# Optimization experiments

Hardware: AMD Instinct MI355X
Metric: run time of the kernel (lower is better)

## Reference

```python
import jax, jax.numpy as jnp
import numpy as np

N = 100000      # total nodes (herb + ingredient + target concatenated)
E = 1600000     # edges (all etypes concatenated)
D_IN = 128
D_HID = 128
D_OUT = 128
BN_EPS = 1e-5
LEAKY_SLOPE = 0.01


def setup_inputs() -> dict:
    key = jax.random.key(0)
    ks = jax.random.split(key, 8)
    x = jax.random.normal(ks[0], (N, D_IN), dtype=jnp.float32)
    src = jax.random.randint(ks[1], (E,), 0, N, dtype=jnp.int32)
    dst = jax.random.randint(ks[2], (E,), 0, N, dtype=jnp.int32)
    W1 = jax.random.normal(ks[3], (D_IN, D_HID), dtype=jnp.float32) * (1.0 / np.sqrt(D_IN))
    b1 = jnp.zeros((D_HID,), jnp.float32)
    W2 = jax.random.normal(ks[4], (D_HID, D_OUT), dtype=jnp.float32) * (1.0 / np.sqrt(D_HID))
    b2 = jnp.zeros((D_OUT,), jnp.float32)
    gamma = jnp.ones((D_HID,), jnp.float32)
    beta = jnp.zeros((D_HID,), jnp.float32)
    run_mean = jax.random.normal(ks[5], (D_HID,), jnp.float32) * 0.1
    run_var = jax.random.uniform(ks[6], (D_HID,), jnp.float32, 0.5, 1.5)
    return {"x": x, "src": src, "dst": dst, "W1": W1, "b1": b1,
            "W2": W2, "b2": b2, "gamma": gamma, "beta": beta,
            "run_mean": run_mean, "run_var": run_var}


def _graph_conv(h, s, d, W, b, norm_src, norm_dst):
    # DGL GraphConv, norm='both': D_out^{-1/2} then sum-aggregate then D_in^{-1/2}, then linear
    h = h * norm_src                                   # [N, d]
    m = jax.ops.segment_sum(h[s], d, num_segments=N)   # gather + spmm-aggregate
    m = m * norm_dst
    return m @ W + b


def reference(x, src, dst, W1, b1, W2, b2, gamma, beta, run_mean, run_var):
    # dgl.add_self_loop: append (i, i) for every node
    loop = jnp.arange(N, dtype=src.dtype)
    s = jnp.concatenate([src, loop])
    d = jnp.concatenate([dst, loop])
    ones = jnp.ones(s.shape[0], jnp.float32)
    out_deg = jnp.maximum(jax.ops.segment_sum(ones, s, num_segments=N), 1.0)
    in_deg = jnp.maximum(jax.ops.segment_sum(ones, d, num_segments=N), 1.0)
    norm_src = (out_deg ** -0.5)[:, None]
    norm_dst = (in_deg ** -0.5)[:, None]

    # layer 0: conv -> BN (eval, running stats) -> leaky_relu -> dropout (eval = identity)
    h = _graph_conv(x, s, d, W1, b1, norm_src, norm_dst)
    h = (h - run_mean) * jax.lax.rsqrt(run_var + BN_EPS) * gamma + beta
    h = jnp.where(h > 0, h, LEAKY_SLOPE * h)

    # layer 1 (last): conv only
    h = _graph_conv(h, s, d, W2, b2, norm_src, norm_dst)
    return h
```

## Files before the change

### kernel.cpp

```cpp
#include <hip/hip_runtime.h>

#define NN 100000
#define NE 1600000
#define D 128
#define LEAKY 0.01f
#define BNEPS 1e-5f

#define G 256
#define CHUNK 6250
#define B 782
#define BSHIFT 7
#define BMASK 127
#define NXCD 8

typedef short v8s __attribute__((ext_vector_type(8)));
typedef float v4f __attribute__((ext_vector_type(4)));

__device__ __forceinline__ unsigned f2bf(float f) {
    unsigned u = __float_as_uint(f);
    return (u + 0x7fffu + ((u >> 16) & 1u)) >> 16;
}
__device__ __forceinline__ float bf2f(unsigned h) {
    return __uint_as_float(h << 16);
}

__device__ __forceinline__ int xcc_id() {
    int x;
    asm volatile("s_getreg_b32 %0, hwreg(HW_REG_XCC_ID)" : "=s"(x));
    return x & (NXCD - 1);
}


__global__ __launch_bounds__(1024) void hist_kernel(const int* __restrict__ src,
                                                    const int* __restrict__ dst,
                                                    int* __restrict__ degP,
                                                    int* __restrict__ hist) {
    __shared__ int h[B];
    for (int i = threadIdx.x; i < B; i += 1024) h[i] = 0;
    __syncthreads();
    int g = blockIdx.x;
    int* dp0 = (int*)(degP) + (size_t)xcc_id() * NN;
    const int* dp = dst + g * CHUNK;
    const int* sp = src + g * CHUNK;
    for (int k = threadIdx.x; k < CHUNK; k += 1024) {
        atomicAdd(&h[dp[k] >> BSHIFT], 1);
        __hip_atomic_fetch_add(&dp0[sp[k]], 1, __ATOMIC_RELAXED,
                               __HIP_MEMORY_SCOPE_WORKGROUP);
    }
    __syncthreads();
    for (int i = threadIdx.x; i < B; i += 1024) hist[i * G + g] = h[i];
}

__global__ void scanA(const int* __restrict__ a, int* __restrict__ bsum) {
    __shared__ int sm[256];
    int t = threadIdx.x;
    sm[t] = a[blockIdx.x * 256 + t];
    __syncthreads();
    for (int s = 128; s > 0; s >>= 1) {
        if (t < s) sm[t] += sm[t + s];
        __syncthreads();
    }
    if (t == 0) bsum[blockIdx.x] = sm[0];
}

__global__ void scanB(const int* __restrict__ bsum, int* __restrict__ boffs) {
    int lane = threadIdx.x;
    int run = 0;
    for (int base = 0; base < B; base += 64) {
        int i = base + lane;
        int v = (i < B) ? bsum[i] : 0;
        int orig = v;
        for (int off = 1; off < 64; off <<= 1) {
            int t = __shfl_up(v, off);
            if (lane >= off) v += t;
        }
        if (i < B) boffs[i] = run + v - orig;
        run += __shfl(v, 63);
    }
}

__global__ void scanC(const int* __restrict__ a, const int* __restrict__ boffs,
                      int* __restrict__ offs) {
    __shared__ int sm[256];
    int t = threadIdx.x;
    int i = blockIdx.x * 256 + t;
    int v = a[i];
    sm[t] = v;
    __syncthreads();
    for (int off = 1; off < 256; off <<= 1) {
        int x = (t >= off) ? sm[t - off] : 0;
        __syncthreads();
        sm[t] += x;
        __syncthreads();
    }
    offs[i] = boffs[blockIdx.x] + sm[t] - v;
}

__global__ __launch_bounds__(1024) void sort_kernel(const int* __restrict__ src,
                                                    const int* __restrict__ dst,
                                                    const int* __restrict__ offs,
                                                    unsigned* __restrict__ ebuf) {
    __shared__ int cur[B];
    int g = blockIdx.x;
    for (int i = threadIdx.x; i < B; i += 1024) cur[i] = offs[i * G + g];
    __syncthreads();
    const int* sp = src + g * CHUNK;
    const int* dp = dst + g * CHUNK;
    for (int k = threadIdx.x; k < CHUNK; k += 1024) {
        int d = dp[k], s = sp[k];
        int pos = atomicAdd(&cur[d >> BSHIFT], 1);
        ebuf[pos] = ((unsigned)(d & BMASK) << 17) | (unsigned)s;
    }
}


__global__ __launch_bounds__(256) void conv_kernel(const float* __restrict__ x,
                                                   const int* __restrict__ degP,
                                                   float* __restrict__ norm_s,
                                                   unsigned* __restrict__ hb) {
    int t = blockIdx.x * 256 + threadIdx.x;
    if (t >= NN * 64) return;
    int row = t >> 6;
    int dsum = 0;
    #pragma unroll
    for (int p = 0; p < NXCD; ++p) dsum += degP[(size_t)p * NN + row];
    float ns = rsqrtf((float)(dsum + 1));
    if ((t & 63) == 0) norm_s[row] = ns;
    float2 v = ((const float2*)x)[t];
    hb[t] = f2bf(v.x * ns) | (f2bf(v.y * ns) << 16);
}


__global__ __launch_bounds__(256) void local_sort(
    const int* __restrict__ offs, unsigned* __restrict__ ebuf,
    int* __restrict__ row, float* __restrict__ norm_d)
{
    __shared__ int cnt[128];
    __shared__ int sc[128];
    const int b = blockIdx.x;
    const int t = threadIdx.x;
    const int s = offs[b * G];
    const int e = (b == B - 1) ? NE : offs[(b + 1) * G];
    if (t < 128) cnt[t] = 0;
    __syncthreads();

    unsigned ent[16];
    int nent = 0;
    for (int k = s + t; k < e && nent < 16; k += 256) {
        unsigned u = ebuf[k];
        ent[nent++] = u;
        atomicAdd(&cnt[u >> 17], 1);
    }
    __syncthreads();

    if (t < 128) sc[t] = cnt[t];
    __syncthreads();
    for (int off = 1; off < 128; off <<= 1) {
        int v = 0;
        if (t < 128 && t >= off) v = sc[t - off];
        __syncthreads();
        if (t < 128) sc[t] += v;
        __syncthreads();
    }
    if (t < 128) {
        int st = s + sc[t] - cnt[t];
        int node = b * 128 + t;
        if (node < NN) {
            row[node] = st;
            norm_d[node] = rsqrtf((float)(cnt[t] + 1));
        }
        cnt[t] = st;
    }
    if (b == B - 1 && t == 0) row[NN] = NE;
    __syncthreads();

    for (int i = 0; i < nent; ++i) {
        unsigned u = ent[i];
        int pos = atomicAdd(&cnt[u >> 17], 1);
        ebuf[pos] = u & 0x1FFFFu;
    }
}


__global__ __launch_bounds__(256) void csr_agg(
    const int* __restrict__ row, const int* __restrict__ csr,
    const unsigned* __restrict__ hp,
    unsigned* __restrict__ Ahi, unsigned* __restrict__ Alo)
{
    int i = blockIdx.x * 4 + (threadIdx.x >> 6);
    if (i >= NN) return;
    int lane = threadIdx.x & 63;

    float2 acc;
    {
        unsigned u = hp[(size_t)i * 64 + lane];
        acc.x = __uint_as_float(u << 16);
        acc.y = __uint_as_float(u & 0xffff0000u);
    }

    int start = row[i], end = row[i + 1];
    for (int base = start; base < end; base += 64) {
        int n = end - base; if (n > 64) n = 64;
        int sv = csr[base + (lane < n ? lane : n - 1)];
        int j = 0;
        for (; j + 8 <= n; j += 8) {
            int ss[8]; unsigned uu[8];
            #pragma unroll
            for (int t = 0; t < 8; ++t) ss[t] = __shfl(sv, j + t);
            #pragma unroll
            for (int t = 0; t < 8; ++t) uu[t] = hp[(size_t)ss[t] * 64 + lane];
            #pragma unroll
            for (int t = 0; t < 8; ++t) {
                acc.x += __uint_as_float(uu[t] << 16);
                acc.y += __uint_as_float(uu[t] & 0xffff0000u);
            }
        }
        for (; j < n; ++j) {
            int s = __shfl(sv, j);
            unsigned u = hp[(size_t)s * 64 + lane];
            acc.x += __uint_as_float(u << 16);
            acc.y += __uint_as_float(u & 0xffff0000u);
        }
    }
    unsigned hx = f2bf(acc.x), hy = f2bf(acc.y);
    float lx = acc.x - bf2f(hx), ly = acc.y - bf2f(hy);
    Ahi[(size_t)i * 64 + lane] = hx | (hy << 16);
    Alo[(size_t)i * 64 + lane] = f2bf(lx) | (f2bf(ly) << 16);
}


template<bool LAYER0>
__global__ __launch_bounds__(256) void gemm_kernel(
    const unsigned* __restrict__ Ahi_g, const unsigned* __restrict__ Alo_g,
    const float* __restrict__ W, const float* __restrict__ bias,
    const float* __restrict__ norm_s, const float* __restrict__ norm_d,
    const float* __restrict__ gamma, const float* __restrict__ beta,
    const float* __restrict__ rmean, const float* __restrict__ rvar,
    float* __restrict__ outf, unsigned short* __restrict__ outb)
{
    __shared__ unsigned lhi[64 * 68];
    __shared__ unsigned llo[64 * 68];

    const int w    = threadIdx.x >> 6;
    const int lane = threadIdx.x & 63;
    const int quad = lane >> 4;
    const int l16  = lane & 15;

    v8s Bhi[2][4], Blo[2][4];
    int col[2];
    #pragma unroll
    for (int ct = 0; ct < 2; ++ct) {
        col[ct] = 32 * w + 16 * ct + l16;
        #pragma unroll
        for (int q = 0; q < 4; ++q) {
            int kb = 32 * q + quad * 8;
            v8s hi8, lo8;
            #pragma unroll
            for (int kk = 0; kk < 8; ++kk) {
                float wv = W[(kb + kk) * D + col[ct]];
                unsigned h = f2bf(wv);
                hi8[kk] = (short)h;
                lo8[kk] = (short)f2bf(wv - bf2f(h));
            }
            Bhi[ct][q] = hi8;
            Blo[ct][q] = lo8;
        }
    }

    float bcol[2], s[2] = {0.f, 0.f}, sh[2] = {0.f, 0.f};
    #pragma unroll
    for (int ct = 0; ct < 2; ++ct) {
        bcol[ct] = bias[col[ct]];
        if (LAYER0) {
            s[ct]  = gamma[col[ct]] * rsqrtf(rvar[col[ct]] + BNEPS);
            sh[ct] = beta[col[ct]] - rmean[col[ct]] * s[ct];
        }
    }

    for (int row0 = blockIdx.x * 64; row0 < NN; row0 += gridDim.x * 64) {
        __syncthreads();
        for (int idx = threadIdx.x; idx < 64 * 64; idx += 256) {
            int r = idx >> 6, cp = idx & 63;
            int rw = row0 + r;
            unsigned vh = 0, vl = 0;
            if (rw < NN) {
                vh = Ahi_g[(size_t)rw * 64 + cp];
                vl = Alo_g[(size_t)rw * 64 + cp];
            }
            lhi[r * 68 + cp] = vh;
            llo[r * 68 + cp] = vl;
        }
        __syncthreads();

        #pragma unroll
        for (int rt = 0; rt < 4; ++rt) {
            v4f acc0 = {0.f, 0.f, 0.f, 0.f};
            v4f acc1 = {0.f, 0.f, 0.f, 0.f};
            #pragma unroll
            for (int q = 0; q < 4; ++q) {
                const unsigned short* ph = (const unsigned short*)lhi
                    + (rt * 16 + l16) * 136 + q * 32 + quad * 8;
                const unsigned short* pl = (const unsigned short*)llo
                    + (rt * 16 + l16) * 136 + q * 32 + quad * 8;
                v8s ahi = *(const v8s*)ph;
                v8s alo = *(const v8s*)pl;
                acc0 = __builtin_amdgcn_mfma_f32_16x16x32_bf16(ahi, Bhi[0][q], acc0, 0, 0, 0);
                acc0 = __builtin_amdgcn_mfma_f32_16x16x32_bf16(alo, Bhi[0][q], acc0, 0, 0, 0);
                acc0 = __builtin_amdgcn_mfma_f32_16x16x32_bf16(ahi, Blo[0][q], acc0, 0, 0, 0);
                acc1 = __builtin_amdgcn_mfma_f32_16x16x32_bf16(ahi, Bhi[1][q], acc1, 0, 0, 0);
                acc1 = __builtin_amdgcn_mfma_f32_16x16x32_bf16(alo, Bhi[1][q], acc1, 0, 0, 0);
                acc1 = __builtin_amdgcn_mfma_f32_16x16x32_bf16(ahi, Blo[1][q], acc1, 0, 0, 0);
            }
            #pragma unroll
            for (int r = 0; r < 4; ++r) {
                int rw = row0 + rt * 16 + quad * 4 + r;
                if (rw >= NN) continue;
                float nd = norm_d[rw];
                float o0 = acc0[r] * nd + bcol[0];
                float o1 = acc1[r] * nd + bcol[1];
                if (LAYER0) {
                    o0 = o0 * s[0] + sh[0];
                    o1 = o1 * s[1] + sh[1];
                    o0 = o0 > 0.f ? o0 : LEAKY * o0;
                    o1 = o1 > 0.f ? o1 : LEAKY * o1;
                    float ns = norm_s[rw];
                    o0 *= ns; o1 *= ns;
                    outb[(size_t)rw * D + col[0]] = (unsigned short)f2bf(o0);
                    outb[(size_t)rw * D + col[1]] = (unsigned short)f2bf(o1);
                } else {
                    outf[(size_t)rw * D + col[0]] = o0;
                    outf[(size_t)rw * D + col[1]] = o1;
                }
            }
        }
    }
}


extern "C" void kernel_launch(void* const* d_in, const int* in_sizes, int n_in,
                              void* d_out, int out_size, void* d_ws, size_t ws_size,
                              hipStream_t stream) {
    const float* x     = (const float*)d_in[0];
    const int*   src   = (const int*)d_in[1];
    const int*   dst   = (const int*)d_in[2];
    const float* W1    = (const float*)d_in[3];
    const float* b1    = (const float*)d_in[4];
    const float* W2    = (const float*)d_in[5];
    const float* b2    = (const float*)d_in[6];
    const float* gamma = (const float*)d_in[7];
    const float* beta  = (const float*)d_in[8];
    const float* rmean = (const float*)d_in[9];
    const float* rvar  = (const float*)d_in[10];
    float* out = (float*)d_out;

    unsigned* hb = (unsigned*)d_out;

    unsigned* Ahi   = (unsigned*)d_ws;
    unsigned* Alo   = Ahi + (size_t)NN * 64;
    float*    norm  = (float*)(Alo + (size_t)NN * 64);
    int*      deg   = (int*)(norm + 2 * NN);
    int*      hist  = deg + NN;
    int*      offs  = hist + B * G;
    int*      bsum  = offs + B * G;
    int*      boffs = bsum + B;
    unsigned* ebuf  = (unsigned*)(boffs + B);
    float* norm_s = norm;
    float* norm_d = norm + NN;
    int*   row    = hist;

    int* degP = (int*)Ahi;

    hipMemsetAsync(degP, 0, (size_t)NXCD * NN * sizeof(int), stream);

    hist_kernel<<<G, 1024, 0, stream>>>(src, dst, degP, hist);
    scanA<<<B * G / 256, 256, 0, stream>>>(hist, bsum);
    scanB<<<1, 64, 0, stream>>>(bsum, boffs);
    scanC<<<B * G / 256, 256, 0, stream>>>(hist, boffs, offs);
    sort_kernel<<<G, 1024, 0, stream>>>(src, dst, offs, ebuf);
    conv_kernel<<<(NN * 64 + 255) / 256, 256, 0, stream>>>(x, degP, norm_s, hb);
    local_sort<<<B, 256, 0, stream>>>(offs, ebuf, row, norm_d);

    const int AGG_BLOCKS = (NN + 3) / 4;
    const int GEMM_BLOCKS = 784;
    csr_agg<<<AGG_BLOCKS, 256, 0, stream>>>(row, (const int*)ebuf, hb, Ahi, Alo);
    gemm_kernel<true><<<GEMM_BLOCKS, 256, 0, stream>>>(Ahi, Alo, W1, b1,
                                                       norm_s, norm_d,
                                                       gamma, beta, rmean, rvar,
                                                       nullptr, (unsigned short*)hb);
    csr_agg<<<AGG_BLOCKS, 256, 0, stream>>>(row, (const int*)ebuf, hb, Ahi, Alo);
    gemm_kernel<false><<<GEMM_BLOCKS, 256, 0, stream>>>(Ahi, Alo, W2, b2,
                                                        norm_s, norm_d,
                                                        nullptr, nullptr, nullptr, nullptr,
                                                        out, nullptr);
}
```

Measured before the change: 454.2 us.

## Fuse CSR aggregation into GEMM kernel, keeping aggregated rows in LDS

Merges the CSR gather-aggregate and the MFMA GEMM into one kernel per layer. Each block aggregates 64 destination rows, with each wave handling 16 rows in sequence, and writes the hi/lo bf16 split straight into shared memory instead of global Ahi/Alo buffers. This removes the global write and re-read of the aggregated matrix and two kernel launches. In exchange, parallelism per row drops (one wave serially handles 16 rows), the per-block W conversion now runs once per 64 rows, and a slow wave with high-degree rows can stall the whole block at the barrier.

```diff
diff --git a/kernel.cpp b/kernel.cpp
--- a/kernel.cpp
+++ b/kernel.cpp
@@ -182,56 +182,10 @@
 }
 
 
-__global__ __launch_bounds__(256) void csr_agg(
-    const int* __restrict__ row, const int* __restrict__ csr,
+template<bool LAYER0>
+__global__ __launch_bounds__(256) void fused_kernel(
+    const int* __restrict__ rowp, const int* __restrict__ csr,
     const unsigned* __restrict__ hp,
-    unsigned* __restrict__ Ahi, unsigned* __restrict__ Alo)
-{
-    int i = blockIdx.x * 4 + (threadIdx.x >> 6);
-    if (i >= NN) return;
-    int lane = threadIdx.x & 63;
-
-    float2 acc;
-    {
-        unsigned u = hp[(size_t)i * 64 + lane];
-        acc.x = __uint_as_float(u << 16);
-        acc.y = __uint_as_float(u & 0xffff0000u);
-    }
-
-    int start = row[i], end = row[i + 1];
-    for (int base = start; base < end; base += 64) {
-        int n = end - base; if (n > 64) n = 64;
-        int sv = csr[base + (lane < n ? lane : n - 1)];
-        int j = 0;
-        for (; j + 8 <= n; j += 8) {
-            int ss[8]; unsigned uu[8];
-            #pragma unroll
-            for (int t = 0; t < 8; ++t) ss[t] = __shfl(sv, j + t);
-            #pragma unroll
-            for (int t = 0; t < 8; ++t) uu[t] = hp[(size_t)ss[t] * 64 + lane];
-            #pragma unroll
-            for (int t = 0; t < 8; ++t) {
-                acc.x += __uint_as_float(uu[t] << 16);
-                acc.y += __uint_as_float(uu[t] & 0xffff0000u);
-            }
-        }
-        for (; j < n; ++j) {
-            int s = __shfl(sv, j);
-            unsigned u = hp[(size_t)s * 64 + lane];
-            acc.x += __uint_as_float(u << 16);
-            acc.y += __uint_as_float(u & 0xffff0000u);
-        }
-    }
-    unsigned hx = f2bf(acc.x), hy = f2bf(acc.y);
-    float lx = acc.x - bf2f(hx), ly = acc.y - bf2f(hy);
-    Ahi[(size_t)i * 64 + lane] = hx | (hy << 16);
-    Alo[(size_t)i * 64 + lane] = f2bf(lx) | (f2bf(ly) << 16);
-}
-
-
-template<bool LAYER0>
-__global__ __launch_bounds__(256) void gemm_kernel(
-    const unsigned* __restrict__ Ahi_g, const unsigned* __restrict__ Alo_g,
     const float* __restrict__ W, const float* __restrict__ bias,
     const float* __restrict__ norm_s, const float* __restrict__ norm_d,
     const float* __restrict__ gamma, const float* __restrict__ beta,
@@ -245,6 +199,7 @@
     const int lane = threadIdx.x & 63;
     const int quad = lane >> 4;
     const int l16  = lane & 15;
+    const int row0 = blockIdx.x * 64;
 
     v8s Bhi[2][4], Blo[2][4];
     int col[2];
@@ -277,60 +232,84 @@
         }
     }
 
-    for (int row0 = blockIdx.x * 64; row0 < NN; row0 += gridDim.x * 64) {
-        __syncthreads();
-        for (int idx = threadIdx.x; idx < 64 * 64; idx += 256) {
-            int r = idx >> 6, cp = idx & 63;
-            int rw = row0 + r;
-            unsigned vh = 0, vl = 0;
-            if (rw < NN) {
-                vh = Ahi_g[(size_t)rw * 64 + cp];
-                vl = Alo_g[(size_t)rw * 64 + cp];
+    for (int k16 = 0; k16 < 16; ++k16) {
+        const int r = w * 16 + k16;
+        const int i = row0 + r;
+        float2 acc = {0.f, 0.f};
+        if (i < NN) {
+            unsigned u = hp[(size_t)i * 64 + lane];
+            acc.x = __uint_as_float(u << 16);
+            acc.y = __uint_as_float(u & 0xffff0000u);
+            int start = rowp[i], end = rowp[i + 1];
+            for (int base = start; base < end; base += 64) {
+                int n = end - base; if (n > 64) n = 64;
+                int sv = csr[base + (lane < n ? lane : n - 1)];
+                int j = 0;
+                for (; j + 8 <= n; j += 8) {
+                    int ss[8]; unsigned uu[8];
+                    #pragma unroll
+                    for (int t = 0; t < 8; ++t) ss[t] = __shfl(sv, j + t);
+                    #pragma unroll
+                    for (int t = 0; t < 8; ++t) uu[t] = hp[(size_t)ss[t] * 64 + lane];
+                    #pragma unroll
+                    for (int t = 0; t < 8; ++t) {
+                        acc.x += __uint_as_float(uu[t] << 16);
+                        acc.y += __uint_as_float(uu[t] & 0xffff0000u);
+                    }
+                }
+                for (; j < n; ++j) {
+                    int sidx = __shfl(sv, j);
+                    unsigned u2 = hp[(size_t)sidx * 64 + lane];
+                    acc.x += __uint_as_float(u2 << 16);
+                    acc.y += __uint_as_float(u2 & 0xffff0000u);
+                }
             }
-            lhi[r * 68 + cp] = vh;
-            llo[r * 68 + cp] = vl;
-        }
-        __syncthreads();
-
+        }
+        unsigned hx = f2bf(acc.x), hy = f2bf(acc.y);
+        float lx = acc.x - bf2f(hx), ly = acc.y - bf2f(hy);
+        lhi[r * 68 + lane] = hx | (hy << 16);
+        llo[r * 68 + lane] = f2bf(lx) | (f2bf(ly) << 16);
+    }
+    __syncthreads();
+
+    #pragma unroll
+    for (int rt = 0; rt < 4; ++rt) {
+        v4f acc0 = {0.f, 0.f, 0.f, 0.f};
+        v4f acc1 = {0.f, 0.f, 0.f, 0.f};
         #pragma unroll
-        for (int rt = 0; rt < 4; ++rt) {
-            v4f acc0 = {0.f, 0.f, 0.f, 0.f};
-            v4f acc1 = {0.f, 0.f, 0.f, 0.f};
-            #pragma unroll
-            for (int q = 0; q < 4; ++q) {
-                const unsigned short* ph = (const unsigned short*)lhi
-                    + (rt * 16 + l16) * 136 + q * 32 + quad * 8;
-                const unsigned short* pl = (const unsigned short*)llo
-                    + (rt * 16 + l16) * 136 + q * 32 + quad * 8;
-                v8s ahi = *(const v8s*)ph;
-                v8s alo = *(const v8s*)pl;
-                acc0 = __builtin_amdgcn_mfma_f32_16x16x32_bf16(ahi, Bhi[0][q], acc0, 0, 0, 0);
-                acc0 = __builtin_amdgcn_mfma_f32_16x16x32_bf16(alo, Bhi[0][q], acc0, 0, 0, 0);
-                acc0 = __builtin_amdgcn_mfma_f32_16x16x32_bf16(ahi, Blo[0][q], acc0, 0, 0, 0);
-                acc1 = __builtin_amdgcn_mfma_f32_16x16x32_bf16(ahi, Bhi[1][q], acc1, 0, 0, 0);
-                acc1 = __builtin_amdgcn_mfma_f32_16x16x32_bf16(alo, Bhi[1][q], acc1, 0, 0, 0);
-                acc1 = __builtin_amdgcn_mfma_f32_16x16x32_bf16(ahi, Blo[1][q], acc1, 0, 0, 0);
-            }
-            #pragma unroll
-            for (int r = 0; r < 4; ++r) {
-                int rw = row0 + rt * 16 + quad * 4 + r;
-                if (rw >= NN) continue;
-                float nd = norm_d[rw];
-                float o0 = acc0[r] * nd + bcol[0];
-                float o1 = acc1[r] * nd + bcol[1];
-                if (LAYER0) {
-                    o0 = o0 * s[0] + sh[0];
-                    o1 = o1 * s[1] + sh[1];
-                    o0 = o0 > 0.f ? o0 : LEAKY * o0;
-                    o1 = o1 > 0.f ? o1 : LEAKY * o1;
-                    float ns = norm_s[rw];
-                    o0 *= ns; o1 *= ns;
-                    outb[(size_t)rw * D + col[0]] = (unsigned short)f2bf(o0);
-                    outb[(size_t)rw * D + col[1]] = (unsigned short)f2bf(o1);
-                } else {
-                    outf[(size_t)rw * D + col[0]] = o0;
-                    outf[(size_t)rw * D + col[1]] = o1;
-                }
+        for (int q = 0; q < 4; ++q) {
+            const unsigned short* ph = (const unsigned short*)lhi
+                + (rt * 16 + l16) * 136 + q * 32 + quad * 8;
+            const unsigned short* pl = (const unsigned short*)llo
+                + (rt * 16 + l16) * 136 + q * 32 + quad * 8;
+            v8s ahi = *(const v8s*)ph;
+            v8s alo = *(const v8s*)pl;
+            acc0 = __builtin_amdgcn_mfma_f32_16x16x32_bf16(ahi, Bhi[0][q], acc0, 0, 0, 0);
+            acc0 = __builtin_amdgcn_mfma_f32_16x16x32_bf16(alo, Bhi[0][q], acc0, 0, 0, 0);
+            acc0 = __builtin_amdgcn_mfma_f32_16x16x32_bf16(ahi, Blo[0][q], acc0, 0, 0, 0);
+            acc1 = __builtin_amdgcn_mfma_f32_16x16x32_bf16(ahi, Bhi[1][q], acc1, 0, 0, 0);
+            acc1 = __builtin_amdgcn_mfma_f32_16x16x32_bf16(alo, Bhi[1][q], acc1, 0, 0, 0);
+            acc1 = __builtin_amdgcn_mfma_f32_16x16x32_bf16(ahi, Blo[1][q], acc1, 0, 0, 0);
+        }
+        #pragma unroll
+        for (int r = 0; r < 4; ++r) {
+            int rw = row0 + rt * 16 + quad * 4 + r;
+            if (rw >= NN) continue;
+            float nd = norm_d[rw];
+            float o0 = acc0[r] * nd + bcol[0];
+            float o1 = acc1[r] * nd + bcol[1];
+            if (LAYER0) {
+                o0 = o0 * s[0] + sh[0];
+                o1 = o1 * s[1] + sh[1];
+                o0 = o0 > 0.f ? o0 : LEAKY * o0;
+                o1 = o1 > 0.f ? o1 : LEAKY * o1;
+                float ns = norm_s[rw];
+                o0 *= ns; o1 *= ns;
+                outb[(size_t)rw * D + col[0]] = (unsigned short)f2bf(o0);
+                outb[(size_t)rw * D + col[1]] = (unsigned short)f2bf(o1);
+            } else {
+                outf[(size_t)rw * D + col[0]] = o0;
+                outf[(size_t)rw * D + col[1]] = o1;
             }
         }
     }
@@ -355,9 +334,9 @@
 
     unsigned* hb = (unsigned*)d_out;
 
-    unsigned* Ahi   = (unsigned*)d_ws;
-    unsigned* Alo   = Ahi + (size_t)NN * 64;
-    float*    norm  = (float*)(Alo + (size_t)NN * 64);
+    unsigned* hs    = (unsigned*)d_ws;
+    unsigned* spare = hs + (size_t)NN * 64;
+    float*    norm  = (float*)(spare + (size_t)NN * 64);
     int*      deg   = (int*)(norm + 2 * NN);
     int*      hist  = deg + NN;
     int*      offs  = hist + B * G;
@@ -368,7 +347,7 @@
     float* norm_d = norm + NN;
     int*   row    = hist;
 
-    int* degP = (int*)Ahi;
+    int* degP = (int*)hs;
 
     hipMemsetAsync(degP, 0, (size_t)NXCD * NN * sizeof(int), stream);
 
@@ -380,16 +359,13 @@
     conv_kernel<<<(NN * 64 + 255) / 256, 256, 0, stream>>>(x, degP, norm_s, hb);
     local_sort<<<B, 256, 0, stream>>>(offs, ebuf, row, norm_d);
 
-    const int AGG_BLOCKS = (NN + 3) / 4;
-    const int GEMM_BLOCKS = 784;
-    csr_agg<<<AGG_BLOCKS, 256, 0, stream>>>(row, (const int*)ebuf, hb, Ahi, Alo);
-    gemm_kernel<true><<<GEMM_BLOCKS, 256, 0, stream>>>(Ahi, Alo, W1, b1,
-                                                       norm_s, norm_d,
-                                                       gamma, beta, rmean, rvar,
-                                                       nullptr, (unsigned short*)hb);
-    csr_agg<<<AGG_BLOCKS, 256, 0, stream>>>(row, (const int*)ebuf, hb, Ahi, Alo);
-    gemm_kernel<false><<<GEMM_BLOCKS, 256, 0, stream>>>(Ahi, Alo, W2, b2,
-                                                        norm_s, norm_d,
-                                                        nullptr, nullptr, nullptr, nullptr,
-                                                        out, nullptr);
-}
+    const int NB = (NN + 63) / 64;
+    fused_kernel<true><<<NB, 256, 0, stream>>>(row, (const int*)ebuf, hb,
+                                               W1, b1, norm_s, norm_d,
+                                               gamma, beta, rmean, rvar,
+                                               nullptr, (unsigned short*)hs);
+    fused_kernel<false><<<NB, 256, 0, stream>>>(row, (const int*)ebuf, hs,
+                                                W2, b2, norm_s, norm_d,
+                                                nullptr, nullptr, nullptr, nullptr,
+                                                out, nullptr);
+}
```

After: 540.5 us. 1.19x slower.
